# Optimization experiments

Measured on AMD Instinct MI355X. Metric: run time of the kernel, lower is better.

## Reference

```python
import jax, jax.numpy as jnp
import numpy as np

G = 64      # num graphs
N = 1024    # nodes per graph (equal-sized graphs)
D_IN, D_H, D_OUT = 128, 256, 10


def setup_inputs() -> dict:
    key = jax.random.key(0)
    k1, k2, k3, k4, k5 = jax.random.split(key, 5)
    x = jax.random.normal(k1, (G * N, D_IN), dtype=jnp.float32)
    batch = jnp.repeat(jnp.arange(G, dtype=jnp.int64), N)  # sorted graph ids
    lim1 = 1.0 / np.sqrt(D_IN)
    lim2 = 1.0 / np.sqrt(D_H)
    W1 = jax.random.uniform(k2, (D_IN, D_H), minval=-lim1, maxval=lim1, dtype=jnp.float32)
    b1 = jax.random.uniform(k3, (D_H,), minval=-lim1, maxval=lim1, dtype=jnp.float32)
    W2 = jax.random.uniform(k4, (D_H, D_OUT), minval=-lim2, maxval=lim2, dtype=jnp.float32)
    b2 = jax.random.uniform(k5, (D_OUT,), minval=-lim2, maxval=lim2, dtype=jnp.float32)
    return {"x": x, "batch": batch, "W1": W1, "b1": b1, "W2": W2, "b2": b2}


def reference(x, batch, W1, b1, W2, b2):
    # Equal-sized graphs: reshape node dim into [G, N, d] (batch is sorted).
    xg = x.reshape(G, N, D_IN)
    # Cosine-similarity adjacency per graph, zero diagonal (from RAW features).
    xn = xg * jax.lax.rsqrt(jnp.sum(xg * xg, axis=-1, keepdims=True) + 1e-24)
    adj = jnp.einsum('gnd,gmd->gnm', xn, xn)            # [G, N, N]
    adj = adj * (1.0 - jnp.eye(N, dtype=adj.dtype))
    # fc1 + relu on node features, then adjacency propagation.
    h = jax.nn.relu(xg @ W1 + b1)                       # [G, N, D_H]
    h = jnp.einsum('gnm,gmd->gnd', adj, h)              # [G, N, D_H]
    # fc2, global mean pool over nodes, log-softmax over classes.
    out = h @ W2 + b2                                   # [G, N, D_OUT]
    pooled = jnp.mean(out, axis=1)                      # [G, D_OUT]
    return jax.nn.log_softmax(pooled, axis=-1)
```

## Files before the change

kernel.cpp:

```cpp
#include <hip/hip_runtime.h>
#include <hip/hip_bf16.h>
#include <string.h>

#define G_ 64
#define N_ 1024
#define DIN 128
#define DH 256
#define DOUT 10

typedef float floatx4 __attribute__((ext_vector_type(4)));
typedef short shortx8 __attribute__((ext_vector_type(8)));

__device__ __forceinline__ ushort f2bf(float f) {
  unsigned u = __builtin_bit_cast(unsigned, f);
  unsigned r = (u + 0x7FFFu + ((u >> 16) & 1u)) >> 16;
  return (ushort)r;
}
__device__ __forceinline__ float bflo(unsigned q) {
  return __builtin_bit_cast(float, q << 16);
}
__device__ __forceinline__ float bfhi(unsigned q) {
  return __builtin_bit_cast(float, q & 0xFFFF0000u);
}

__global__ __launch_bounds__(256) void k0_w1t(
    const float* __restrict__ W1, ushort* __restrict__ w1t) {
  const int idx = blockIdx.x * 256 + threadIdx.x;
  const int k = idx >> 8, d = idx & 255;
  w1t[d * DIN + k] = f2bf(W1[k * DH + d]);
}

__global__ __launch_bounds__(256) void k1_norm_u(
    const float* __restrict__ x, float* __restrict__ norminv,
    float* __restrict__ u, ushort* __restrict__ xb) {
  const int g = blockIdx.x >> 4;
  const int wave = threadIdx.x >> 6;
  const int lane = threadIdx.x & 63;
  __shared__ float red[4][DIN];
  float a0 = 0.f, a1 = 0.f;
  const int mbase = blockIdx.x * 64 + wave * 16;
  for (int i = 0; i < 16; ++i) {
    const int m = mbase + i;
    const float2 v = ((const float2*)(x + (size_t)m * DIN))[lane];
    float ss = v.x * v.x + v.y * v.y;
    #pragma unroll
    for (int off = 32; off; off >>= 1) ss += __shfl_xor(ss, off, 64);
    const float ninv = rsqrtf(ss + 1e-24f);
    if (lane == 0) norminv[m] = ninv;
    ((unsigned*)xb)[(size_t)m * (DIN / 2) + lane] =
        (unsigned)f2bf(v.x) | ((unsigned)f2bf(v.y) << 16);
    a0 = fmaf(v.x, ninv, a0);
    a1 = fmaf(v.y, ninv, a1);
  }
  red[wave][2 * lane] = a0;
  red[wave][2 * lane + 1] = a1;
  __syncthreads();
  if (threadIdx.x < DIN) {
    const float t = red[0][threadIdx.x] + red[1][threadIdx.x] +
                    red[2][threadIdx.x] + red[3][threadIdx.x];
    atomicAdd(&u[g * DIN + threadIdx.x], t);
  }
}

__global__ __launch_bounds__(256) void k2_mfma(
    const ushort* __restrict__ xb, const ushort* __restrict__ w1t,
    const float* __restrict__ b1, const float* __restrict__ norminv,
    const float* __restrict__ u, float* __restrict__ hw) {
  const int g = blockIdx.x >> 3;
  const int mb = (blockIdx.x & 7) << 7;
  const int lane = threadIdx.x & 63;
  const int wave = threadIdx.x >> 6;
  const int quad = lane >> 4;
  const int l16 = lane & 15;
  __shared__ float u_lds[DIN];
  __shared__ float s_lds[128];

  if (threadIdx.x < DIN) u_lds[threadIdx.x] = u[g * DIN + threadIdx.x];
  __syncthreads();

  {
    const int nd = threadIdx.x >> 1;
    const int half = threadIdx.x & 1;
    const size_t m = (size_t)(g << 10) + mb + nd;
    const uint4* xr = (const uint4*)(xb + m * DIN + half * 64);
    float p = 0.f;
    #pragma unroll
    for (int j = 0; j < 8; ++j) {
      const uint4 q = xr[j];
      const float* ub = &u_lds[half * 64 + j * 8];
      p = fmaf(bflo(q.x), ub[0], p); p = fmaf(bfhi(q.x), ub[1], p);
      p = fmaf(bflo(q.y), ub[2], p); p = fmaf(bfhi(q.y), ub[3], p);
      p = fmaf(bflo(q.z), ub[4], p); p = fmaf(bfhi(q.z), ub[5], p);
      p = fmaf(bflo(q.w), ub[6], p); p = fmaf(bfhi(q.w), ub[7], p);
    }
    p += __shfl_xor(p, 1, 64);
    if (!half) s_lds[nd] = p * norminv[m] - 1.0f;
  }
  __syncthreads();

  shortx8 bfr[4][4];
  #pragma unroll
  for (int dt = 0; dt < 4; ++dt) {
    const int d = (wave << 6) + (dt << 4) + l16;
    #pragma unroll
    for (int kt = 0; kt < 4; ++kt)
      bfr[dt][kt] = *(const shortx8*)(w1t + (size_t)d * DIN + (kt << 5) + (quad << 3));
  }
  float b1v[4];
  #pragma unroll
  for (int dt = 0; dt < 4; ++dt) b1v[dt] = b1[(wave << 6) + (dt << 4) + l16];

  float wsum[4] = {0.f, 0.f, 0.f, 0.f};
  for (int mt = 0; mt < 8; ++mt) {
    const ushort* ar = xb + ((size_t)(g << 10) + mb + (mt << 4) + l16) * DIN;
    shortx8 af[4];
    #pragma unroll
    for (int kt = 0; kt < 4; ++kt)
      af[kt] = *(const shortx8*)(ar + (kt << 5) + (quad << 3));

    floatx4 acc[4] = {{0.f, 0.f, 0.f, 0.f}, {0.f, 0.f, 0.f, 0.f},
                      {0.f, 0.f, 0.f, 0.f}, {0.f, 0.f, 0.f, 0.f}};
    #pragma unroll
    for (int kt = 0; kt < 4; ++kt)
      #pragma unroll
      for (int dt = 0; dt < 4; ++dt)
        acc[dt] = __builtin_amdgcn_mfma_f32_16x16x32_bf16(af[kt], bfr[dt][kt],
                                                          acc[dt], 0, 0, 0);
    #pragma unroll
    for (int dt = 0; dt < 4; ++dt) {
      float bs = 0.f;
      #pragma unroll
      for (int r = 0; r < 4; ++r) {
        const float h = fmaxf(acc[dt][r] + b1v[dt], 0.f);
        bs = fmaf(s_lds[(mt << 4) + (quad << 2) + r], h, bs);
      }
      wsum[dt] += bs;
    }
  }
  #pragma unroll
  for (int dt = 0; dt < 4; ++dt) {
    float w = wsum[dt];
    w += __shfl_xor(w, 16, 64);
    w += __shfl_xor(w, 32, 64);
    if (quad == 0)
      atomicAdd(&hw[g * DH + (wave << 6) + (dt << 4) + l16], w);
  }
}

__global__ __launch_bounds__(64) void k3_head(
    const float* __restrict__ hw, const float* __restrict__ W2,
    const float* __restrict__ b2, float* __restrict__ out) {
  const int g = blockIdx.x;
  const int t = threadIdx.x;
  __shared__ float partial[40];
  __shared__ float p[DOUT];
  if (t < 40) {
    const int c = t % 10, q = t / 10;
    const float* hg = hw + g * DH + q * 64;
    float a = 0.f;
    #pragma unroll
    for (int k = 0; k < 64; ++k) a = fmaf(hg[k], W2[(q * 64 + k) * DOUT + c], a);
    partial[t] = a;
  }
  __syncthreads();
  if (t < DOUT) {
    p[t] = (partial[t] + partial[t + 10] + partial[t + 20] + partial[t + 30]) *
               (1.0f / N_) + b2[t];
  }
  __syncthreads();
  if (t < DOUT) {
    float mx = p[0];
    #pragma unroll
    for (int c = 1; c < DOUT; ++c) mx = fmaxf(mx, p[c]);
    float se = 0.f;
    #pragma unroll
    for (int c = 0; c < DOUT; ++c) se += expf(p[c] - mx);
    out[g * DOUT + t] = p[t] - (mx + logf(se));
  }
}

extern "C" void kernel_launch(void* const* d_in, const int* in_sizes, int n_in,
                              void* d_out, int out_size, void* d_ws, size_t ws_size,
                              hipStream_t stream) {
  const float* x  = (const float*)d_in[0];
  const float* W1 = (const float*)d_in[2];
  const float* b1 = (const float*)d_in[3];
  const float* W2 = (const float*)d_in[4];
  const float* b2 = (const float*)d_in[5];
  float* out = (float*)d_out;

  float* hw = (float*)d_ws;
  float* u  = hw + G_ * DH;
  float* norminv = u + G_ * DIN;
  ushort* xb  = (ushort*)(norminv + G_ * N_);
  ushort* w1t = xb + (size_t)G_ * N_ * DIN;

  hipMemsetAsync(d_ws, 0, (size_t)(G_ * DH + G_ * DIN) * sizeof(float), stream);
  k0_w1t<<<DIN, 256, 0, stream>>>(W1, w1t);
  k1_norm_u<<<G_ * 16, 256, 0, stream>>>(x, norminv, u, xb);
  k2_mfma<<<G_ * 8, 256, 0, stream>>>(xb, w1t, b1, norminv, u, hw);
  k3_head<<<G_, 64, 0, stream>>>(hw, W2, b2, out);
}
```

Before: 111.3 us.

## Fuse five launches into two kernels with last-block head reduction

```diff
diff --git a/kernel.cpp b/kernel.cpp
--- a/kernel.cpp
+++ b/kernel.cpp
@@ -1,6 +1,4 @@
 #include <hip/hip_runtime.h>
-#include <hip/hip_bf16.h>
-#include <string.h>
 
 #define G_ 64
 #define N_ 1024
@@ -23,24 +21,28 @@
   return __builtin_bit_cast(float, q & 0xFFFF0000u);
 }
 
-__global__ __launch_bounds__(256) void k0_w1t(
-    const float* __restrict__ W1, ushort* __restrict__ w1t) {
-  const int idx = blockIdx.x * 256 + threadIdx.x;
-  const int k = idx >> 8, d = idx & 255;
-  w1t[d * DIN + k] = f2bf(W1[k * DH + d]);
-}
-
-__global__ __launch_bounds__(256) void k1_norm_u(
-    const float* __restrict__ x, float* __restrict__ norminv,
-    float* __restrict__ u, ushort* __restrict__ xb) {
-  const int g = blockIdx.x >> 4;
-  const int wave = threadIdx.x >> 6;
-  const int lane = threadIdx.x & 63;
+__global__ __launch_bounds__(256) void kA(
+    const float* __restrict__ x, const float* __restrict__ W1,
+    ushort* __restrict__ xb, ushort* __restrict__ w1t,
+    float* __restrict__ u_part, float* __restrict__ norminv,
+    int* __restrict__ cnt) {
+  const int bid = blockIdx.x;
+  const int tid = threadIdx.x;
+  const int wave = tid >> 6;
+  const int lane = tid & 63;
+  const int m0 = bid << 7;
+
   __shared__ float red[4][DIN];
+
+  if (bid == 0 && tid < G_) cnt[tid] = 0;
+
+  if (bid < DIN)
+    w1t[(size_t)tid * DIN + bid] = f2bf(W1[(size_t)bid * DH + tid]);
+
   float a0 = 0.f, a1 = 0.f;
-  const int mbase = blockIdx.x * 64 + wave * 16;
-  for (int i = 0; i < 16; ++i) {
-    const int m = mbase + i;
+  for (int i = 0; i < 32; ++i) {
+    const int nb = (wave << 5) + i;
+    const int m = m0 + nb;
     const float2 v = ((const float2*)(x + (size_t)m * DIN))[lane];
     float ss = v.x * v.x + v.y * v.y;
     #pragma unroll
@@ -55,34 +57,43 @@
   red[wave][2 * lane] = a0;
   red[wave][2 * lane + 1] = a1;
   __syncthreads();
-  if (threadIdx.x < DIN) {
-    const float t = red[0][threadIdx.x] + red[1][threadIdx.x] +
-                    red[2][threadIdx.x] + red[3][threadIdx.x];
-    atomicAdd(&u[g * DIN + threadIdx.x], t);
-  }
-}
-
-__global__ __launch_bounds__(256) void k2_mfma(
+  if (tid < DIN)
+    u_part[bid * DIN + tid] =
+        red[0][tid] + red[1][tid] + red[2][tid] + red[3][tid];
+}
+
+__global__ __launch_bounds__(256) void kB(
     const ushort* __restrict__ xb, const ushort* __restrict__ w1t,
-    const float* __restrict__ b1, const float* __restrict__ norminv,
-    const float* __restrict__ u, float* __restrict__ hw) {
-  const int g = blockIdx.x >> 3;
-  const int mb = (blockIdx.x & 7) << 7;
-  const int lane = threadIdx.x & 63;
-  const int wave = threadIdx.x >> 6;
-  const int quad = lane >> 4;
-  const int l16 = lane & 15;
+    const float* __restrict__ b1, const float* __restrict__ W2,
+    const float* __restrict__ b2, const float* __restrict__ u_part,
+    const float* __restrict__ norminv, float* __restrict__ hw_part,
+    int* __restrict__ cnt, float* __restrict__ out) {
+  const int bid = blockIdx.x;
+  const int tid = threadIdx.x;
+  const int wave = tid >> 6;
+  const int lane = tid & 63;
+  const int g = bid >> 3;
+  const int m0 = bid << 7;
+
   __shared__ float u_lds[DIN];
   __shared__ float s_lds[128];
-
-  if (threadIdx.x < DIN) u_lds[threadIdx.x] = u[g * DIN + threadIdx.x];
+  __shared__ float hv[DH];
+  __shared__ float partial[40];
+  __shared__ float pv[DOUT];
+  __shared__ int lastflag;
+
+  if (tid < DIN) {
+    float s = 0.f;
+    #pragma unroll
+    for (int i = 0; i < 8; ++i) s += u_part[((g << 3) + i) * DIN + tid];
+    u_lds[tid] = s;
+  }
   __syncthreads();
 
   {
-    const int nd = threadIdx.x >> 1;
-    const int half = threadIdx.x & 1;
-    const size_t m = (size_t)(g << 10) + mb + nd;
-    const uint4* xr = (const uint4*)(xb + m * DIN + half * 64);
+    const int nd = tid >> 1;
+    const int half = tid & 1;
+    const uint4* xr = (const uint4*)(xb + ((size_t)m0 + nd) * DIN + half * 64);
     float p = 0.f;
     #pragma unroll
     for (int j = 0; j < 8; ++j) {
@@ -94,9 +105,12 @@
       p = fmaf(bflo(q.w), ub[6], p); p = fmaf(bfhi(q.w), ub[7], p);
     }
     p += __shfl_xor(p, 1, 64);
-    if (!half) s_lds[nd] = p * norminv[m] - 1.0f;
-  }
-  __syncthreads();
+    if (!half) s_lds[nd] = p * norminv[m0 + nd] - 1.0f;
+  }
+  __syncthreads();
+
+  const int quad = lane >> 4;
+  const int l16 = lane & 15;
 
   shortx8 bfr[4][4];
   #pragma unroll
@@ -104,7 +118,8 @@
     const int d = (wave << 6) + (dt << 4) + l16;
     #pragma unroll
     for (int kt = 0; kt < 4; ++kt)
-      bfr[dt][kt] = *(const shortx8*)(w1t + (size_t)d * DIN + (kt << 5) + (quad << 3));
+      bfr[dt][kt] =
+          *(const shortx8*)(w1t + (size_t)d * DIN + (kt << 5) + (quad << 3));
   }
   float b1v[4];
   #pragma unroll
@@ -112,7 +127,7 @@
 
   float wsum[4] = {0.f, 0.f, 0.f, 0.f};
   for (int mt = 0; mt < 8; ++mt) {
-    const ushort* ar = xb + ((size_t)(g << 10) + mb + (mt << 4) + l16) * DIN;
+    const ushort* ar = xb + ((size_t)m0 + (mt << 4) + l16) * DIN;
     shortx8 af[4];
     #pragma unroll
     for (int kt = 0; kt < 4; ++kt)
@@ -143,39 +158,43 @@
     w += __shfl_xor(w, 16, 64);
     w += __shfl_xor(w, 32, 64);
     if (quad == 0)
-      atomicAdd(&hw[g * DH + (wave << 6) + (dt << 4) + l16], w);
-  }
-}
-
-__global__ __launch_bounds__(64) void k3_head(
-    const float* __restrict__ hw, const float* __restrict__ W2,
-    const float* __restrict__ b2, float* __restrict__ out) {
-  const int g = blockIdx.x;
-  const int t = threadIdx.x;
-  __shared__ float partial[40];
-  __shared__ float p[DOUT];
-  if (t < 40) {
-    const int c = t % 10, q = t / 10;
-    const float* hg = hw + g * DH + q * 64;
+      hw_part[bid * DH + (wave << 6) + (dt << 4) + l16] = w;
+  }
+
+  __syncthreads();
+  __threadfence();
+  if (tid == 0) lastflag = (atomicAdd(&cnt[g], 1) == 7);
+  __syncthreads();
+  if (!lastflag) return;
+  __threadfence();
+
+  float h = 0.f;
+  #pragma unroll
+  for (int i = 0; i < 8; ++i) h += hw_part[((g << 3) + i) * DH + tid];
+  hv[tid] = h;
+  __syncthreads();
+  if (tid < 40) {
+    const int c = tid % 10, q = tid / 10;
     float a = 0.f;
     #pragma unroll
-    for (int k = 0; k < 64; ++k) a = fmaf(hg[k], W2[(q * 64 + k) * DOUT + c], a);
-    partial[t] = a;
-  }
-  __syncthreads();
-  if (t < DOUT) {
-    p[t] = (partial[t] + partial[t + 10] + partial[t + 20] + partial[t + 30]) *
-               (1.0f / N_) + b2[t];
-  }
-  __syncthreads();
-  if (t < DOUT) {
-    float mx = p[0];
-    #pragma unroll
-    for (int c = 1; c < DOUT; ++c) mx = fmaxf(mx, p[c]);
+    for (int k = 0; k < 64; ++k)
+      a = fmaf(hv[q * 64 + k], W2[(q * 64 + k) * DOUT + c], a);
+    partial[tid] = a;
+  }
+  __syncthreads();
+  if (tid < DOUT) {
+    pv[tid] = (partial[tid] + partial[tid + 10] + partial[tid + 20] +
+               partial[tid + 30]) * (1.0f / N_) + b2[tid];
+  }
+  __syncthreads();
+  if (tid < DOUT) {
+    float mx = pv[0];
+    #pragma unroll
+    for (int c = 1; c < DOUT; ++c) mx = fmaxf(mx, pv[c]);
     float se = 0.f;
     #pragma unroll
-    for (int c = 0; c < DOUT; ++c) se += expf(p[c] - mx);
-    out[g * DOUT + t] = p[t] - (mx + logf(se));
+    for (int c = 0; c < DOUT; ++c) se += expf(pv[c] - mx);
+    out[g * DOUT + tid] = pv[tid] - (mx + logf(se));
   }
 }
 
@@ -189,15 +208,14 @@
   const float* b2 = (const float*)d_in[5];
   float* out = (float*)d_out;
 
-  float* hw = (float*)d_ws;
-  float* u  = hw + G_ * DH;
-  float* norminv = u + G_ * DIN;
-  ushort* xb  = (ushort*)(norminv + G_ * N_);
+  ushort* xb  = (ushort*)d_ws;
   ushort* w1t = xb + (size_t)G_ * N_ * DIN;
-
-  hipMemsetAsync(d_ws, 0, (size_t)(G_ * DH + G_ * DIN) * sizeof(float), stream);
-  k0_w1t<<<DIN, 256, 0, stream>>>(W1, w1t);
-  k1_norm_u<<<G_ * 16, 256, 0, stream>>>(x, norminv, u, xb);
-  k2_mfma<<<G_ * 8, 256, 0, stream>>>(xb, w1t, b1, norminv, u, hw);
-  k3_head<<<G_, 64, 0, stream>>>(hw, W2, b2, out);
-}
+  float* u_part  = (float*)(w1t + (size_t)DH * DIN);
+  float* hw_part = u_part + (size_t)512 * DIN;
+  float* norminv = hw_part + (size_t)512 * DH;
+  int* cnt = (int*)(norminv + (size_t)G_ * N_);
+
+  kA<<<512, 256, 0, stream>>>(x, W1, xb, w1t, u_part, norminv, cnt);
+  kB<<<512, 256, 0, stream>>>(xb, w1t, b1, W2, b2, u_part, norminv, hw_part,
+                              cnt, out);
+}
```

Result: slower. 161.3 us (+44.9%).
